# Performance work log

Hardware: AMD Instinct MI355X
Metric: run time of the kernel (lower is better)

The kernel has to match this reference:

```python
import jax, jax.numpy as jnp
import numpy as np
from jax import lax

MAX_OBJ = 100
IOU_THRES = 0.45
SCORE_THRES = 0.25
MAX_WH = 7680.0

# xywh -> xyxy conversion matrix (same as ONNX_ORT.convert_matrix)
CONVERT = jnp.array([[1, 0, 1, 0],
                     [0, 1, 0, 1],
                     [-0.5, 0, 0.5, 0],
                     [0, -0.5, 0, 0.5]], dtype=jnp.float32)


def _iou_one_vs_all(box, boxes):
    # box: [4] xyxy, boxes: [N,4] xyxy
    x1 = jnp.maximum(box[0], boxes[:, 0])
    y1 = jnp.maximum(box[1], boxes[:, 1])
    x2 = jnp.minimum(box[2], boxes[:, 2])
    y2 = jnp.minimum(box[3], boxes[:, 3])
    inter = jnp.clip(x2 - x1, 0.0) * jnp.clip(y2 - y1, 0.0)
    a = (box[2] - box[0]) * (box[3] - box[1])
    b = (boxes[:, 2] - boxes[:, 0]) * (boxes[:, 3] - boxes[:, 1])
    return inter / (a + b - inter + 1e-9)


def _nms_indices(nmsbox, max_score):
    # Greedy class-offset NMS; returns [MAX_OBJ] indices, -1 for padding.
    valid0 = max_score >= SCORE_THRES

    def step(valid, _):
        s = jnp.where(valid, max_score, -1.0)
        i = jnp.argmax(s)
        ok = s[i] >= SCORE_THRES
        iou = _iou_one_vs_all(nmsbox[i], nmsbox)
        valid = valid & (iou <= IOU_THRES)
        valid = valid.at[i].set(False)
        return valid, jnp.where(ok, i, -1)

    _, idxs = lax.scan(step, valid0, None, length=MAX_OBJ)
    return idxs


def _forward(x1, x2, num_labels1, num_labels2):
    B, N1, _ = x1.shape
    N2 = x2.shape[1]
    # pad x1 class scores with zeros for model2's labels (appended at end)
    x1p = jnp.concatenate([x1, jnp.zeros((B, N1, num_labels2), x1.dtype)], axis=2)
    # pad x2: insert zeros for model1's labels between conf and its own classes
    x2p = jnp.concatenate([x2[:, :, 0:5],
                           jnp.zeros((B, N2, num_labels1), x2.dtype),
                           x2[:, :, 5:]], axis=2)
    x = jnp.concatenate([x1p, x2p], axis=1)  # [B, N1+N2, 5+C1+C2]

    boxes = x[:, :, :4] @ CONVERT            # xywh -> xyxy, [B,N,4]
    conf = x[:, :, 4:5]
    scores = x[:, :, 5:] * conf              # [B,N,C]
    max_score = scores.max(axis=2)           # [B,N]
    cat_id = scores.argmax(axis=2)           # [B,N]
    # class-offset boxes so NMS is class-aware
    nmsbox = boxes + cat_id[..., None].astype(boxes.dtype) * MAX_WH

    idxs = jax.vmap(_nms_indices)(lax.stop_gradient(nmsbox),
                                  lax.stop_gradient(max_score))  # [B,MAX_OBJ]
    mask = idxs >= 0
    si = jnp.maximum(idxs, 0)
    sel_boxes = jnp.take_along_axis(boxes, si[..., None], axis=1)      # [B,MAX_OBJ,4]
    sel_cat = jnp.take_along_axis(cat_id, si, axis=1).astype(boxes.dtype)
    sel_score = jnp.take_along_axis(max_score, si, axis=1)

    mf = mask.astype(boxes.dtype)
    Xcol = jnp.where(mask, jnp.arange(B)[:, None], -1).astype(boxes.dtype)
    out = jnp.concatenate([Xcol[..., None],
                           sel_boxes * mf[..., None],
                           (sel_cat * mf)[..., None],
                           (sel_score * mf)[..., None]], axis=2)
    return out.reshape(B * MAX_OBJ, 7)


def setup_inputs() -> dict:
    key = jax.random.key(0)
    k1, k2 = jax.random.split(key)
    x1 = jax.random.uniform(k1, (4, 25200, 85), dtype=jnp.float32)
    x2 = jax.random.uniform(k2, (4, 25200, 25), dtype=jnp.float32)
    return {"x1": x1, "x2": x2, "num_labels1": 80, "num_labels2": 20}


def reference(x1, x2, num_labels1, num_labels2):
    return _forward(x1, x2, num_labels1, num_labels2)
```

## Files before the change

### kernel.cpp

```cpp
#include <hip/hip_runtime.h>
#include <stdint.h>

#pragma clang fp contract(off)

#define BATCH 4
#define N1 25200
#define NROW 50400
#define NCLS 100
#define TOT (BATCH*NROW)
#define CAPB 1280
#define SCORE_T 0.25f
#define IOU_T 0.45f
#define MAXWH 7680.0f

#define X1_SLAB 64
#define X1_SPB 394
#define X2_SLAB 256
#define X2_SPB 99

#define BIN_SLICES 128
#define BIN_SL 394

typedef unsigned long long u64;

__device__ __forceinline__ u64 pack_key(unsigned sb, int n, int cid) {
    return ((u64)sb << 32) | ((u64)(unsigned)((n ^ 0xFFFF) & 0xFFFF) << 8) | (u64)(unsigned)cid;
}

__device__ __forceinline__ bool sup_test(float inter, float sum) {
    float d = (sum - inter) + 1e-9f;
    float t1 = IOU_T * d;
    bool hi = inter > t1 * 1.00001f;
    bool lo = inter < t1 * 0.99999f;
    if (__builtin_expect(!(hi || lo), 0)) return (inter / d) > IOU_T;
    return hi;
}

__device__ __forceinline__ float rl(float v, int srcLane) {
    return __int_as_float(__builtin_amdgcn_readlane(__float_as_int(v), srcLane));
}

__device__ __forceinline__ void blk2bucket(int blk, int& b, int& c) {
    if (blk < BATCH * 20) { b = blk / 20; c = 80 + (blk - b * 20); }
    else { int z = blk - BATCH * 20; b = z / 80; c = z - b * 80; }
}

__device__ __forceinline__ int prefix_ge(const u64* list, int cnt, u64 T) {
    int lo = 0, hi = cnt;
    while (lo < hi) {
        int mid = (lo + hi) >> 1;
        if (list[mid] >= T) lo = mid + 1; else hi = mid;
    }
    return lo;
}

__device__ __forceinline__ void sort_desc(u64* sk, int L, int t) {
    bool act = (t * 8) < L;
    u64 r[8];
    if (act) {
#pragma unroll
        for (int e = 0; e < 8; ++e) r[e] = sk[t * 8 + e];
    }
    for (int k = 2; k <= L; k <<= 1) {
        for (int j = k >> 1; j > 0; j >>= 1) {
            if (j >= 512) {
                if (act) {
#pragma unroll
                    for (int e = 0; e < 8; ++e) sk[t * 8 + e] = r[e];
                }
                __syncthreads();
                if (act) {
                    bool iAmLo = (t & (j >> 3)) == 0;
                    bool descSeg = (t & (k >> 3)) == 0;
                    bool takeMax = (descSeg == iAmLo);
#pragma unroll
                    for (int e = 0; e < 8; ++e) {
                        u64 u = r[e];
                        u64 v = sk[(t * 8 + e) ^ j];
                        bool uGE = (u >= v);
                        r[e] = (takeMax == uGE) ? u : v;
                    }
                }
                __syncthreads();
            } else if (j >= 8) {
                if (act) {
                    int dt = j >> 3;
                    bool iAmLo = (t & dt) == 0;
                    bool descSeg = (t & (k >> 3)) == 0;
                    bool takeMax = (descSeg == iAmLo);
#pragma unroll
                    for (int e = 0; e < 8; ++e) {
                        u64 u = r[e];
                        u64 v = __shfl_xor(u, dt, 64);
                        bool uGE = (u >= v);
                        r[e] = (takeMax == uGE) ? u : v;
                    }
                }
            } else {
                if (act) {
#pragma unroll
                    for (int e = 0; e < 8; ++e) {
                        if (!(e & j)) {
                            int e2 = e | j;
                            bool descSeg = (k >= 8) ? ((t & (k >> 3)) == 0)
                                                    : ((e & k) == 0);
                            u64 lo = r[e], hi = r[e2];
                            bool sw = descSeg ? (lo < hi) : (lo > hi);
                            if (sw) { r[e] = hi; r[e2] = lo; }
                        }
                    }
                }
            }
        }
    }
    if (act) {
#pragma unroll
        for (int e = 0; e < 8; ++e) sk[t * 8 + e] = r[e];
    }
    __syncthreads();
}

__global__ __launch_bounds__(256) void k_rows(const float* __restrict__ x1,
                                              const float* __restrict__ x2,
                                              float4* __restrict__ boxes4,
                                              u64* __restrict__ rowKey) {
    __shared__ float4 ld4[1600];
    float* ld = (float*)ld4;
    int blk = blockIdx.x;
    int t = threadIdx.x;
    const int NX1 = BATCH * X1_SPB;
    if (blk < NX1) {
        int b = blk / X1_SPB, s = blk - b * X1_SPB;
        int r0 = s * X1_SLAB;
        int nr = min(X1_SLAB, N1 - r0);
        const float4* src = (const float4*)(x1 + ((size_t)b * N1 + r0) * 85);
        int count4 = (nr * 85) >> 2;
        for (int i = t; i < count4; i += 256) ld4[i] = src[i];
        __syncthreads();
        int row = t >> 2, sub = t & 3;
        if (row < nr) {
            const float* p = ld + row * 85;
            float conf = p[4];
            u64 key = 0ULL;
            int base = sub * 20;
            for (int c = 0; c < 20; ++c) {
                int j = base + c;
                float v = p[5 + j] * conf;
                u64 kk = ((u64)__float_as_uint(v) << 32) | (unsigned)~(unsigned)j;
                if (kk > key) key = kk;
            }
            u64 o;
            o = __shfl_xor(key, 1, 64); if (o > key) key = o;
            o = __shfl_xor(key, 2, 64); if (o > key) key = o;
            if (sub == 0) {
                float best = __uint_as_float((unsigned)(key >> 32));
                int bestj = ~(unsigned)key;
                int n = r0 + row;
                int r = b * NROW + n;
                u64 outk = 0ULL;
                if (best >= SCORE_T) {
                    float cx = p[0], cy = p[1], w = p[2], h = p[3];
                    boxes4[r] = make_float4(cx - 0.5f * w, cy - 0.5f * h,
                                            cx + 0.5f * w, cy + 0.5f * h);
                    outk = pack_key((unsigned)(key >> 32), n, bestj);
                }
                rowKey[r] = outk;
            }
        }
    } else {
        int blk2 = blk - NX1;
        int b = blk2 / X2_SPB, s = blk2 - b * X2_SPB;
        int r0 = s * X2_SLAB;
        int nr = min(X2_SLAB, N1 - r0);
        const float4* src = (const float4*)(x2 + ((size_t)b * N1 + r0) * 25);
        int count4 = (nr * 25) >> 2;
        for (int i = t; i < count4; i += 256) ld4[i] = src[i];
        __syncthreads();
        if (t < nr) {
            const float* p = ld + t * 25;
            float conf = p[4];
            float best = 0.0f; int bestj = 0;
            for (int j2 = 0; j2 < 20; ++j2) {
                float v = p[5 + j2] * conf;
                if (v > best) { best = v; bestj = 80 + j2; }
            }
            int n = N1 + r0 + t;
            int r = b * NROW + n;
            u64 outk = 0ULL;
            if (best >= SCORE_T) {
                float cx = p[0], cy = p[1], w = p[2], h = p[3];
                boxes4[r] = make_float4(cx - 0.5f * w, cy - 0.5f * h,
                                        cx + 0.5f * w, cy + 0.5f * h);
                outk = pack_key(__float_as_uint(best), n, bestj);
            }
            rowKey[r] = outk;
        }
    }
}

__global__ __launch_bounds__(256) void k_bin(const u64* __restrict__ rowKey,
                                             u64* __restrict__ csrKey,
                                             int* __restrict__ fill) {
    __shared__ u64 keys[BIN_SL];
    __shared__ int cnt[NCLS];
    __shared__ int base[NCLS];
    __shared__ int cur[NCLS];
    int blk = blockIdx.x;
    int b = blk / BIN_SLICES, s = blk - b * BIN_SLICES;
    int r0 = s * BIN_SL;
    int nr = min(BIN_SL, NROW - r0);
    int t = threadIdx.x;
    if (t < NCLS) { cnt[t] = 0; cur[t] = 0; }
    __syncthreads();
    const u64* src = rowKey + (size_t)b * NROW + r0;
    for (int i = t; i < nr; i += 256) {
        u64 k = src[i];
        keys[i] = k;
        if (k != 0ULL) atomicAdd(&cnt[(int)(k & 0xFF)], 1);
    }
    __syncthreads();
    if (t < NCLS && cnt[t] > 0)
        base[t] = atomicAdd(&fill[b * NCLS + t], cnt[t]);
    __syncthreads();
    for (int i = t; i < nr; i += 256) {
        u64 k = keys[i];
        if (k != 0ULL) {
            int c = (int)(k & 0xFF);
            int p = base[c] + atomicAdd(&cur[c], 1);
            if (p < CAPB) csrKey[(size_t)(b * NCLS + c) * CAPB + p] = k;
        }
    }
}

__global__ __launch_bounds__(256) void k_sort(u64* __restrict__ csrKey,
                                              const int* __restrict__ fill,
                                              int* __restrict__ accCnt) {
    __shared__ u64 sk[2048];
    int b, c; blk2bucket(blockIdx.x, b, c);
    int bucket = b * NCLS + c;
    int t = threadIdx.x;
    int cnt0 = min(fill[bucket], CAPB);
    if (cnt0 == 0) { if (t == 0) accCnt[bucket] = 0; return; }
    u64* src = csrKey + (size_t)bucket * CAPB;
    int L = 512; while (L < cnt0) L <<= 1;
    for (int i = t; i < L; i += 256) sk[i] = (i < cnt0) ? src[i] : 0ULL;
    __syncthreads();
    sort_desc(sk, L, t);
    for (int i = t; i < cnt0; i += 256) src[i] = sk[i];
}

__global__ __launch_bounds__(64) void k_greedy(const float4* __restrict__ boxes4,
                                               const u64* __restrict__ csrKey,
                                               const int* __restrict__ fill,
                                               u64* __restrict__ accKey,
                                               int* __restrict__ accCnt) {
    __shared__ float4 accQ[100];
    __shared__ float accA[100];
    int b, c; blk2bucket(blockIdx.x, b, c);
    int bucket = b * NCLS + c;
    int lane = threadIdx.x;
    int cnt0 = min(fill[bucket], CAPB);
    if (cnt0 == 0) { if (lane == 0) accCnt[bucket] = 0; return; }
    const u64* skB = csrKey + (size_t)bucket * CAPB;
    float off = (float)c * MAXWH;
    int m = 0;
    for (int base = 0; base < cnt0 && m < 100; base += 64) {
        int j = base + lane;
        bool alive = (j < cnt0);
        float4 a = make_float4(0.f, 0.f, 0.f, 0.f);
        float aA = 0.f; u64 myKey = 0ULL;
        if (alive) {
            myKey = skB[j];
            int n = 0xFFFF ^ (int)((myKey >> 8) & 0xFFFF);
            a = boxes4[b * NROW + n];
            a.x += off; a.y += off; a.z += off; a.w += off;
            aA = (a.z - a.x) * (a.w - a.y);
        }
        int k2 = 0;
        while (k2 < m) {
            if (__ballot(alive) == 0ULL) break;
            int rem = m - k2;
            if (rem >= 8) {
#pragma unroll
                for (int u = 0; u < 8; ++u) {
                    float4 q = accQ[k2 + u];
                    float qa = accA[k2 + u];
                    float xx1 = fmaxf(a.x, q.x), yy1 = fmaxf(a.y, q.y);
                    float xx2 = fminf(a.z, q.z), yy2 = fminf(a.w, q.w);
                    float inter = fmaxf(xx2 - xx1, 0.f) * fmaxf(yy2 - yy1, 0.f);
                    alive = alive && !sup_test(inter, qa + aA);
                }
                k2 += 8;
            } else {
                for (int u = 0; u < rem; ++u) {
                    float4 q = accQ[k2 + u];
                    float qa = accA[k2 + u];
                    float xx1 = fmaxf(a.x, q.x), yy1 = fmaxf(a.y, q.y);
                    float xx2 = fminf(a.z, q.z), yy2 = fminf(a.w, q.w);
                    float inter = fmaxf(xx2 - xx1, 0.f) * fmaxf(yy2 - yy1, 0.f);
                    alive = alive && !sup_test(inter, qa + aA);
                }
                k2 = m;
            }
        }
        u64 av = __ballot(alive);
        int accIdx = -1;
        while (av != 0ULL && m < 100) {
            int f = __builtin_ctzll(av);
            float qx = rl(a.x, f), qy = rl(a.y, f);
            float qz = rl(a.z, f), qw = rl(a.w, f);
            if (lane == f) { accIdx = m; alive = false; }
            ++m;
            if (alive) {
                float qa = (qz - qx) * (qw - qy);
                float xx1 = fmaxf(a.x, qx), yy1 = fmaxf(a.y, qy);
                float xx2 = fminf(a.z, qz), yy2 = fminf(a.w, qw);
                float inter = fmaxf(xx2 - xx1, 0.f) * fmaxf(yy2 - yy1, 0.f);
                alive = !sup_test(inter, qa + aA);
            }
            av = __ballot(alive);
        }
        if (accIdx >= 0) {
            accQ[accIdx] = a; accA[accIdx] = aA;
            accKey[(size_t)bucket * 100 + accIdx] = myKey;
        }
    }
    if (lane == 0) accCnt[bucket] = m;
}

__global__ __launch_bounds__(256) void k_merge(const float4* __restrict__ boxes4,
                                               const u64* __restrict__ accKey,
                                               const int* __restrict__ accCnt,
                                               float* __restrict__ out) {
    __shared__ u64 sk[1024];
    __shared__ u64 head[NCLS];
    __shared__ int cnts[NCLS];
    __shared__ int pc[NCLS];
    int b = blockIdx.x, t = threadIdx.x;
    const u64* base = accKey + (size_t)b * NCLS * 100;
    if (t < NCLS) {
        int cc = accCnt[b * NCLS + t];
        cnts[t] = cc;
        head[t] = (cc > 0) ? base[t * 100] : 0ULL;
    }
    __syncthreads();
    int S = 0, ne = 0; u64 mn = ~0ULL;
    for (int c = 0; c < NCLS; ++c) {
        int cc = cnts[c];
        S += cc;
        if (cc > 0) { ++ne; u64 h = head[c]; if (h < mn) mn = h; }
    }
    u64 T;
    bool bisect;
    if (S <= 900)            { T = 0ULL; bisect = false; }
    else if (ne == NCLS)     { T = mn;   bisect = false; }
    else                     { T = 0ULL; bisect = true;  }
    if (t < NCLS) pc[t] = bisect ? 0 : prefix_ge(base + t * 100, cnts[t], T);
    __syncthreads();
    int G = 0;
    for (int c = 0; c < NCLS; ++c) G += pc[c];
    if (G > 1000) bisect = true;
    if (bisect) {
        u64 lo = 0ULL, hi = ~0ULL;
        for (int it = 0; it < 64; ++it) {
            u64 mid = lo + ((hi - lo) >> 1);
            if (t < NCLS) pc[t] = prefix_ge(base + t * 100, cnts[t], mid);
            __syncthreads();
            int cnt = 0;
            for (int c = 0; c < NCLS; ++c) cnt += pc[c];
            if (cnt >= 100 && cnt <= 1000) { T = mid; G = cnt; break; }
            if (cnt < 100) hi = mid; else lo = mid;
            __syncthreads();
        }
    }
    if (t < NCLS) {
        int off = 0;
        for (int c = 0; c < t; ++c) off += pc[c];
        int p = pc[t];
        for (int j = 0; j < p; ++j) sk[off + j] = base[t * 100 + j];
    }
    for (int i = G + t; i < 1024; i += 256) sk[i] = 0ULL;
    __syncthreads();
    sort_desc(sk, 1024, t);
    if (t < 100) {
        u64 k = sk[t];
        float* o7 = out + (size_t)(b * 100 + t) * 7;
        if (k == 0ULL) {
            o7[0] = -1.0f;
            o7[1] = 0.0f; o7[2] = 0.0f; o7[3] = 0.0f;
            o7[4] = 0.0f; o7[5] = 0.0f; o7[6] = 0.0f;
        } else {
            int n = 0xFFFF ^ (int)((k >> 8) & 0xFFFF);
            int cid = (int)(k & 0xFF);
            float4 bx = boxes4[b * NROW + n];
            o7[0] = (float)b;
            o7[1] = bx.x; o7[2] = bx.y; o7[3] = bx.z; o7[4] = bx.w;
            o7[5] = (float)cid;
            o7[6] = __uint_as_float((unsigned)(k >> 32));
        }
    }
}

extern "C" void kernel_launch(void* const* d_in, const int* in_sizes, int n_in,
                              void* d_out, int out_size, void* d_ws, size_t ws_size,
                              hipStream_t stream) {
    const float* x1 = (const float*)d_in[0];
    const float* x2 = (const float*)d_in[1];
    float* out = (float*)d_out;

    float4* boxes4 = (float4*)d_ws;
    u64* rowKey = (u64*)(boxes4 + TOT);
    u64* csrKey = rowKey + TOT;
    u64* accKey = csrKey + (size_t)BATCH * NCLS * CAPB;
    int* fill   = (int*)(accKey + (size_t)BATCH * NCLS * 100);
    int* accCnt = fill + BATCH * NCLS;

    hipMemsetAsync(fill, 0, sizeof(int) * BATCH * NCLS, stream);

    int rowBlocks = BATCH * X1_SPB + BATCH * X2_SPB;
    k_rows<<<rowBlocks, 256, 0, stream>>>(x1, x2, boxes4, rowKey);
    k_bin<<<BATCH * BIN_SLICES, 256, 0, stream>>>(rowKey, csrKey, fill);
    k_sort<<<BATCH * NCLS, 256, 0, stream>>>(csrKey, fill, accCnt);
    k_greedy<<<BATCH * NCLS, 64, 0, stream>>>(boxes4, csrKey, fill, accKey, accCnt);
    k_merge<<<BATCH, 256, 0, stream>>>(boxes4, accKey, accCnt, out);
}
```

Baseline: 137.4 us.

## Prefetch next candidate chunk in greedy NMS and unroll slab loads

The greedy NMS kernel now loads the next 64-candidate chunk's keys and boxes while the current chunk is tested against accepted boxes, hiding the dependent global-load latency behind suppression work. The row kernels also replace the strided copy loop with fully unrolled independent float4 loads for full slabs, so more memory requests are in flight at once. This costs extra registers, and the prefetch may load data that is never used once 100 boxes have been accepted.

```diff
diff --git a/kernel.cpp b/kernel.cpp
--- a/kernel.cpp
+++ b/kernel.cpp
@@ -135,7 +135,18 @@
         int nr = min(X1_SLAB, N1 - r0);
         const float4* src = (const float4*)(x1 + ((size_t)b * N1 + r0) * 85);
         int count4 = (nr * 85) >> 2;
-        for (int i = t; i < count4; i += 256) ld4[i] = src[i];
+        if (count4 == 1360) {
+            float4 v0 = src[t], v1 = src[t + 256], v2 = src[t + 512];
+            float4 v3 = src[t + 768], v4 = src[t + 1024];
+            float4 v5;
+            bool h5 = (t < 80);
+            if (h5) v5 = src[t + 1280];
+            ld4[t] = v0; ld4[t + 256] = v1; ld4[t + 512] = v2;
+            ld4[t + 768] = v3; ld4[t + 1024] = v4;
+            if (h5) ld4[t + 1280] = v5;
+        } else {
+            for (int i = t; i < count4; i += 256) ld4[i] = src[i];
+        }
         __syncthreads();
         int row = t >> 2, sub = t & 3;
         if (row < nr) {
@@ -174,7 +185,18 @@
         int nr = min(X2_SLAB, N1 - r0);
         const float4* src = (const float4*)(x2 + ((size_t)b * N1 + r0) * 25);
         int count4 = (nr * 25) >> 2;
-        for (int i = t; i < count4; i += 256) ld4[i] = src[i];
+        if (count4 == 1600) {
+            float4 v0 = src[t], v1 = src[t + 256], v2 = src[t + 512];
+            float4 v3 = src[t + 768], v4 = src[t + 1024], v5 = src[t + 1280];
+            float4 v6;
+            bool h6 = (t < 64);
+            if (h6) v6 = src[t + 1536];
+            ld4[t] = v0; ld4[t + 256] = v1; ld4[t + 512] = v2;
+            ld4[t + 768] = v3; ld4[t + 1024] = v4; ld4[t + 1280] = v5;
+            if (h6) ld4[t + 1536] = v6;
+        } else {
+            for (int i = t; i < count4; i += 256) ld4[i] = src[i];
+        }
         __syncthreads();
         if (t < nr) {
             const float* p = ld + t * 25;
@@ -263,19 +285,22 @@
     if (cnt0 == 0) { if (lane == 0) accCnt[bucket] = 0; return; }
     const u64* skB = csrKey + (size_t)bucket * CAPB;
     float off = (float)c * MAXWH;
+    u64 curKey = (lane < cnt0) ? skB[lane] : 0ULL;
+    float4 curBox = make_float4(0.f, 0.f, 0.f, 0.f);
+    if (lane < cnt0) {
+        int n = 0xFFFF ^ (int)((curKey >> 8) & 0xFFFF);
+        curBox = boxes4[b * NROW + n];
+    }
     int m = 0;
     for (int base = 0; base < cnt0 && m < 100; base += 64) {
         int j = base + lane;
         bool alive = (j < cnt0);
-        float4 a = make_float4(0.f, 0.f, 0.f, 0.f);
-        float aA = 0.f; u64 myKey = 0ULL;
-        if (alive) {
-            myKey = skB[j];
-            int n = 0xFFFF ^ (int)((myKey >> 8) & 0xFFFF);
-            a = boxes4[b * NROW + n];
-            a.x += off; a.y += off; a.z += off; a.w += off;
-            aA = (a.z - a.x) * (a.w - a.y);
-        }
+        u64 myKey = curKey;
+        float4 a = curBox;
+        a.x += off; a.y += off; a.z += off; a.w += off;
+        float aA = (a.z - a.x) * (a.w - a.y);
+        int jn = j + 64;
+        u64 nk = (jn < cnt0) ? skB[jn] : 0ULL;
         int k2 = 0;
         while (k2 < m) {
             if (__ballot(alive) == 0ULL) break;
@@ -302,6 +327,11 @@
                 }
                 k2 = m;
             }
+        }
+        float4 nb = make_float4(0.f, 0.f, 0.f, 0.f);
+        if (jn < cnt0) {
+            int nn = 0xFFFF ^ (int)((nk >> 8) & 0xFFFF);
+            nb = boxes4[b * NROW + nn];
         }
         u64 av = __ballot(alive);
         int accIdx = -1;
@@ -324,6 +354,7 @@
             accQ[accIdx] = a; accA[accIdx] = aA;
             accKey[(size_t)bucket * 100 + accIdx] = myKey;
         }
+        curKey = nk; curBox = nb;
     }
     if (lane == 0) accCnt[bucket] = m;
 }
```

Result: no change. 136.7 us (-0.5%).
